# Kernel tuning notes

Measured on AMD Instinct MI355X. Metric: run time of the kernel, lower is better.

Reference implementation:

```python
import jax, jax.numpy as jnp
import numpy as np

N_QUBITS = 4
DIM = 2 ** N_QUBITS  # 16-dim statevector
KERNEL = 3
STRIDE = 1
PADDING = 1


def _rot_mats(w):
    # PennyLane Rot(phi, theta, omega) = RZ(omega) RY(theta) RZ(phi)
    phi, theta, omega = w[:, 0], w[:, 1], w[:, 2]
    c = jnp.cos(theta / 2)
    s = jnp.sin(theta / 2)
    em = jnp.exp(-0.5j * (phi + omega))
    ep = jnp.exp(0.5j * (phi + omega))
    ed = jnp.exp(0.5j * (phi - omega))
    edm = jnp.exp(-0.5j * (phi - omega))
    row0 = jnp.stack([em * c, -ed * s], axis=-1)
    row1 = jnp.stack([edm * s, ep * c], axis=-1)
    return jnp.stack([row0, row1], axis=-2)  # [n_qubits, 2, 2]


def _apply_1q(state, U, wire):
    # state: [M] + [2]*n, wire axis is 1+wire (wire 0 is most significant)
    s = jnp.moveaxis(state, 1 + wire, -1)
    s = jnp.einsum('...b,ab->...a', s, U)
    return jnp.moveaxis(s, -1, 1 + wire)


def _apply_cnot(state, c, t):
    s = jnp.moveaxis(state, (1 + c, 1 + t), (-2, -1))
    shp = s.shape
    s = s.reshape(shp[:-2] + (4,))[..., jnp.array([0, 1, 3, 2])].reshape(shp)
    return jnp.moveaxis(s, (-2, -1), (1 + c, 1 + t))


def _forward(x, W_pre, b_pre, W_post, b_post, q_weights):
    B, C, L = x.shape
    xp = jnp.pad(x, ((0, 0), (0, 0), (PADDING, PADDING)))
    L_out = (L + 2 * PADDING - KERNEL) // STRIDE + 1
    starts = jnp.arange(L_out) * STRIDE
    # windows: [B, C, L_out, K] -> flatten channel-major like torch reshape
    win = xp[:, :, starts[:, None] + jnp.arange(KERNEL)[None, :]]
    win = win.transpose(0, 2, 1, 3).reshape(B, L_out, C * KERNEL)
    pre = win @ W_pre.T + b_pre  # [B, L_out, n_qubits]
    # AmplitudeEmbedding: pad to 2**n and normalize
    v = jnp.pad(pre, ((0, 0), (0, 0), (0, DIM - N_QUBITS)))
    v = v / jnp.linalg.norm(v, axis=-1, keepdims=True)
    state = v.reshape(B * L_out, *([2] * N_QUBITS)).astype(jnp.complex64)
    U = _rot_mats(q_weights)
    for i in range(N_QUBITS):
        state = _apply_1q(state, U[i], i)
    for i in range(N_QUBITS - 1):
        state = _apply_cnot(state, i, i + 1)
    flat = state.reshape(B * L_out, DIM)
    probs = jnp.real(flat) ** 2 + jnp.imag(flat) ** 2
    # PauliZ expectation per wire: sign of bit i (wire 0 = MSB)
    bits = (jnp.arange(DIM)[None, :] >> (N_QUBITS - 1 - jnp.arange(N_QUBITS)[:, None])) & 1
    z = (1 - 2 * bits).astype(probs.dtype)  # [n_qubits, DIM]
    expz = (probs @ z.T).reshape(B, L_out, N_QUBITS)
    out = expz @ W_post.T + b_post  # [B, L_out, out_channels]
    return out.transpose(0, 2, 1)


def setup_inputs() -> dict:
    key = jax.random.key(0)
    ks = jax.random.split(key, 6)
    B, C, L = 32, 80, 3000
    OUT = 512
    return {
        'x': jax.random.normal(ks[0], (B, C, L), dtype=jnp.float32),
        'W_pre': jax.random.normal(ks[1], (N_QUBITS, C * KERNEL), dtype=jnp.float32) * 0.06,
        'b_pre': jax.random.normal(ks[2], (N_QUBITS,), dtype=jnp.float32) * 0.06,
        'W_post': jax.random.normal(ks[3], (OUT, N_QUBITS), dtype=jnp.float32) * 0.4,
        'b_post': jax.random.normal(ks[4], (OUT,), dtype=jnp.float32) * 0.4,
        'q_weights': jax.random.normal(ks[5], (N_QUBITS, 3), dtype=jnp.float32),
    }


def reference(x, W_pre, b_pre, W_post, b_post, q_weights):
    return _forward(x, W_pre, b_pre, W_post, b_post, q_weights)
```

## Files before the change

### kernel.cpp

```cpp
#include <hip/hip_runtime.h>
#include <math.h>

#define C_IN 80
#define L_IN 3000
#define OUT_C 512
#define TL1 128
#define NT1 256
#define NT2 256
#define TL2 256
#define OH  256

struct c2f { float x, y; };

__device__ __forceinline__ c2f cmul(c2f a, c2f b) {
    return { a.x*b.x - a.y*b.y, a.x*b.y + a.y*b.x };
}
__device__ __forceinline__ c2f csel(c2f a, c2f b, int bit) {
    c2f r; r.x = bit ? b.x : a.x; r.y = bit ? b.y : a.y; return r;
}
__device__ __forceinline__ float quadform(const float4* __restrict__ A, float4 p) {
    float4 r0 = A[0], r1 = A[1], r2 = A[2], r3 = A[3];
    return p.x*(r0.x*p.x + r0.y*p.y + r0.z*p.z + r0.w*p.w)
         + p.y*(r1.x*p.x + r1.y*p.y + r1.z*p.z + r1.w*p.w)
         + p.z*(r2.x*p.x + r2.y*p.y + r2.z*p.z + r2.w*p.w)
         + p.w*(r3.x*p.x + r3.y*p.y + r3.z*p.z + r3.w*p.w);
}

__global__ __launch_bounds__(NT1) void qconv_expz_kernel(
    const float* __restrict__ x,
    const float* __restrict__ W_pre,
    const float* __restrict__ b_pre,
    const float* __restrict__ qw,
    float4* __restrict__ expz)
{
    __shared__ float4 s_wpre[C_IN*3];
    __shared__ float4 s_A[4][4];
    __shared__ float4 s_part[TL1];

    const int t  = threadIdx.x;
    const int b  = blockIdx.y;
    const int l0 = blockIdx.x * TL1;

    for (int i = t; i < C_IN*3; i += NT1) {
        s_wpre[i] = make_float4(W_pre[0*C_IN*3 + i], W_pre[1*C_IN*3 + i],
                                W_pre[2*C_IN*3 + i], W_pre[3*C_IN*3 + i]);
    }
    __syncthreads();

    if (t < 64) {
        c2f U[4][2][2];
        #pragma unroll
        for (int i = 0; i < 4; ++i) {
            float phi = qw[i*3+0], theta = qw[i*3+1], omega = qw[i*3+2];
            float sh, ch;  sincosf(0.5f*theta, &sh, &ch);
            float s1, c1;  sincosf(0.5f*(phi+omega), &s1, &c1);
            float s2, cv;  sincosf(0.5f*(phi-omega), &s2, &cv);
            U[i][0][0] = {  c1*ch, -s1*ch };
            U[i][0][1] = { -cv*sh, -s2*sh };
            U[i][1][0] = {  cv*sh, -s2*sh };
            U[i][1][1] = {  c1*ch,  s1*ch };
        }
        const int q  = t >> 4;
        const int j  = (t >> 2) & 3;
        const int jp = t & 3;
        const int j2  = (j  >> 1) & 1, j3  = j  & 1;
        const int jp2 = (jp >> 1) & 1, jp3 = jp & 1;
        float s = 0.f;
        #pragma unroll
        for (int k = 0; k < 16; ++k) {
            int m = k ^ ((k >> 1) & 1);
            m ^= ((m >> 2) & 1) << 1;
            m ^= ((m >> 3) & 1) << 2;
            const int m0 = (m >> 3) & 1, m1 = (m >> 2) & 1;
            const int m2 = (m >> 1) & 1, m3 = m & 1;
            c2f w01 = cmul(U[0][m0][0], U[1][m1][0]);
            c2f av = cmul(w01, cmul(csel(U[2][m2][0], U[2][m2][1], j2),
                                    csel(U[3][m3][0], U[3][m3][1], j3)));
            c2f bv = cmul(w01, cmul(csel(U[2][m2][0], U[2][m2][1], jp2),
                                    csel(U[3][m3][0], U[3][m3][1], jp3)));
            float z = 1.f - 2.f * ((k >> (3 - q)) & 1);
            s += z * (av.x*bv.x + av.y*bv.y);
        }
        ((float*)s_A)[t] = s;
    }

    const int i = t & (TL1 - 1);
    const int h = t >> 7;
    const int l = l0 + i;
    const bool lvalid = (l < L_IN);

    float4 acc = (h == 0) ? make_float4(b_pre[0], b_pre[1], b_pre[2], b_pre[3])
                          : make_float4(0.f, 0.f, 0.f, 0.f);
    if (lvalid) {
        const float* __restrict__ xrow = x + (size_t)b * C_IN * L_IN + (size_t)(h*40) * L_IN + l;
        const bool has_m1 = (l >= 1);
        const bool has_p1 = (l + 1 < L_IN);
        #pragma unroll 4
        for (int c = 0; c < 40; ++c) {
            const float* r = xrow + c * L_IN;
            float xa = has_m1 ? r[-1] : 0.f;
            float xb = r[0];
            float xc = has_p1 ? r[1] : 0.f;
            float4 w0 = s_wpre[(h*40+c)*3+0], w1 = s_wpre[(h*40+c)*3+1], w2 = s_wpre[(h*40+c)*3+2];
            acc.x += w0.x*xa + w1.x*xb + w2.x*xc;
            acc.y += w0.y*xa + w1.y*xb + w2.y*xc;
            acc.z += w0.z*xa + w1.z*xb + w2.z*xc;
            acc.w += w0.w*xa + w1.w*xb + w2.w*xc;
        }
    }
    if (h == 1) s_part[i] = acc;
    __syncthreads();

    if (t < TL1 && lvalid) {
        float4 p = acc;
        float4 q2 = s_part[t];
        p.x += q2.x; p.y += q2.y; p.z += q2.z; p.w += q2.w;
        const float inv = 1.f / (p.x*p.x + p.y*p.y + p.z*p.z + p.w*p.w);
        float4 e;
        e.x = quadform(s_A[0], p) * inv;
        e.y = quadform(s_A[1], p) * inv;
        e.z = quadform(s_A[2], p) * inv;
        e.w = quadform(s_A[3], p) * inv;
        expz[(size_t)b * L_IN + l] = e;
    }
}

__global__ __launch_bounds__(NT2) void expand_kernel(
    const float4* __restrict__ expz,
    const float* __restrict__ W_post,
    const float* __restrict__ b_post,
    float* __restrict__ out)
{
    __shared__ float4 s_post[OH];
    __shared__ float  s_bpost[OH];

    const int t  = threadIdx.x;
    const int b  = blockIdx.z;
    const int oh = blockIdx.y;
    const int l0 = blockIdx.x * TL2;

    const int obase = oh * OH;
    s_post[t]  = *reinterpret_cast<const float4*>(&W_post[(obase + t) * 4]);
    s_bpost[t] = b_post[obase + t];

    const int lane = t & 63;
    const int w    = t >> 6;
    const int l    = l0 + 4 * lane;
    const bool v   = (l + 3 < L_IN);

    float4 e0, e1, e2, e3;
    if (v) {
        const float4* ep = expz + (size_t)b * L_IN + l;
        e0 = ep[0]; e1 = ep[1]; e2 = ep[2]; e3 = ep[3];
    }
    __syncthreads();
    if (!v) return;

    float* op = out + (size_t)b * OUT_C * L_IN + (size_t)(obase + w) * L_IN + l;
    #pragma unroll 8
    for (int k = 0; k < OH/4; ++k) {
        const int o = w + 4*k;
        const float4 wv = s_post[o];
        const float  bb = s_bpost[o];
        float4 st;
        st.x = wv.x*e0.x + wv.y*e0.y + wv.z*e0.z + wv.w*e0.w + bb;
        st.y = wv.x*e1.x + wv.y*e1.y + wv.z*e1.z + wv.w*e1.w + bb;
        st.z = wv.x*e2.x + wv.y*e2.y + wv.z*e2.z + wv.w*e2.w + bb;
        st.w = wv.x*e3.x + wv.y*e3.y + wv.z*e3.z + wv.w*e3.w + bb;
        *reinterpret_cast<float4*>(op) = st;
        op += (size_t)4 * L_IN;
    }
}

extern "C" void kernel_launch(void* const* d_in, const int* in_sizes, int n_in,
                              void* d_out, int out_size, void* d_ws, size_t ws_size,
                              hipStream_t stream) {
    const float* x      = (const float*)d_in[0];
    const float* W_pre  = (const float*)d_in[1];
    const float* b_pre  = (const float*)d_in[2];
    const float* W_post = (const float*)d_in[3];
    const float* b_post = (const float*)d_in[4];
    const float* qw     = (const float*)d_in[5];
    float* out = (float*)d_out;
    float4* expz = (float4*)d_ws;

    const int B = in_sizes[0] / (C_IN * L_IN);
    dim3 grid1((L_IN + TL1 - 1) / TL1, B);
    qconv_expz_kernel<<<grid1, NT1, 0, stream>>>(x, W_pre, b_pre, qw, expz);
    dim3 grid2((L_IN + TL2 - 1) / TL2, OUT_C / OH, B);
    expand_kernel<<<grid2, NT2, 0, stream>>>(expz, W_post, b_post, out);
}
```

Measured before the change: 49.42 us.

## Restructure expand kernel to stage full expz row in LDS with register-held weights

The expand kernel now gives each block 32 output channels for one batch. It loads the whole batch row of expz (3000 float4, 48KB) into shared memory, and each wave keeps 8 weight rows and biases in registers. Every wave sweeps the full length and writes 8 output rows per iteration. This removes the per-element shared-memory weight reads and the remainder handling. In exchange it uses 48KB of LDS per block, which lowers occupancy, and 3000 (not a multiple of 4) relies on the l<L_IN guard for the last float4.

```diff
diff --git a/kernel.cpp b/kernel.cpp
--- a/kernel.cpp
+++ b/kernel.cpp
@@ -7,8 +7,8 @@
 #define TL1 128
 #define NT1 256
 #define NT2 256
-#define TL2 256
-#define OH  256
+
+typedef float floatx4 __attribute__((ext_vector_type(4)));
 
 struct c2f { float x, y; };
 
@@ -34,7 +34,7 @@
     float4* __restrict__ expz)
 {
     __shared__ float4 s_wpre[C_IN*3];
-    __shared__ float4 s_A[4][4];
+    __shared__ float4 s_A[16];
     __shared__ float4 s_part[TL1];
 
     const int t  = threadIdx.x;
@@ -117,10 +117,10 @@
         p.x += q2.x; p.y += q2.y; p.z += q2.z; p.w += q2.w;
         const float inv = 1.f / (p.x*p.x + p.y*p.y + p.z*p.z + p.w*p.w);
         float4 e;
-        e.x = quadform(s_A[0], p) * inv;
-        e.y = quadform(s_A[1], p) * inv;
-        e.z = quadform(s_A[2], p) * inv;
-        e.w = quadform(s_A[3], p) * inv;
+        e.x = quadform(&s_A[0],  p) * inv;
+        e.y = quadform(&s_A[4],  p) * inv;
+        e.z = quadform(&s_A[8],  p) * inv;
+        e.w = quadform(&s_A[12], p) * inv;
         expz[(size_t)b * L_IN + l] = e;
     }
 }
@@ -131,44 +131,45 @@
     const float* __restrict__ b_post,
     float* __restrict__ out)
 {
-    __shared__ float4 s_post[OH];
-    __shared__ float  s_bpost[OH];
+    __shared__ float4 s_e[L_IN];
 
-    const int t  = threadIdx.x;
-    const int b  = blockIdx.z;
-    const int oh = blockIdx.y;
-    const int l0 = blockIdx.x * TL2;
+    const int t    = threadIdx.x;
+    const int og   = blockIdx.x;
+    const int b    = blockIdx.y;
+    const int w    = t >> 6;
+    const int lane = t & 63;
 
-    const int obase = oh * OH;
-    s_post[t]  = *reinterpret_cast<const float4*>(&W_post[(obase + t) * 4]);
-    s_bpost[t] = b_post[obase + t];
+    const float4* ep = expz + (size_t)b * L_IN;
+    for (int i = t; i < L_IN; i += NT2) s_e[i] = ep[i];
 
-    const int lane = t & 63;
-    const int w    = t >> 6;
-    const int l    = l0 + 4 * lane;
-    const bool v   = (l + 3 < L_IN);
-
-    float4 e0, e1, e2, e3;
-    if (v) {
-        const float4* ep = expz + (size_t)b * L_IN + l;
-        e0 = ep[0]; e1 = ep[1]; e2 = ep[2]; e3 = ep[3];
+    const int obase = og*32 + w*8;
+    float4 wv[8]; float bb[8];
+    #pragma unroll
+    for (int r = 0; r < 8; ++r) {
+        wv[r] = *reinterpret_cast<const float4*>(&W_post[(obase + r) * 4]);
+        bb[r] = b_post[obase + r];
     }
     __syncthreads();
-    if (!v) return;
 
-    float* op = out + (size_t)b * OUT_C * L_IN + (size_t)(obase + w) * L_IN + l;
-    #pragma unroll 8
-    for (int k = 0; k < OH/4; ++k) {
-        const int o = w + 4*k;
-        const float4 wv = s_post[o];
-        const float  bb = s_bpost[o];
-        float4 st;
-        st.x = wv.x*e0.x + wv.y*e0.y + wv.z*e0.z + wv.w*e0.w + bb;
-        st.y = wv.x*e1.x + wv.y*e1.y + wv.z*e1.z + wv.w*e1.w + bb;
-        st.z = wv.x*e2.x + wv.y*e2.y + wv.z*e2.z + wv.w*e2.w + bb;
-        st.w = wv.x*e3.x + wv.y*e3.y + wv.z*e3.z + wv.w*e3.w + bb;
-        *reinterpret_cast<float4*>(op) = st;
-        op += (size_t)4 * L_IN;
+    float* orow = out + ((size_t)b * OUT_C + obase) * L_IN;
+    #pragma unroll 2
+    for (int it = 0; it < (L_IN + 255) / 256; ++it) {
+        const int l = it*256 + lane*4;
+        if (l < L_IN) {
+            const float4 e0 = s_e[l+0];
+            const float4 e1 = s_e[l+1];
+            const float4 e2 = s_e[l+2];
+            const float4 e3 = s_e[l+3];
+            #pragma unroll
+            for (int r = 0; r < 8; ++r) {
+                floatx4 st;
+                st.x = wv[r].x*e0.x + wv[r].y*e0.y + wv[r].z*e0.z + wv[r].w*e0.w + bb[r];
+                st.y = wv[r].x*e1.x + wv[r].y*e1.y + wv[r].z*e1.z + wv[r].w*e1.w + bb[r];
+                st.z = wv[r].x*e2.x + wv[r].y*e2.y + wv[r].z*e2.z + wv[r].w*e2.w + bb[r];
+                st.w = wv[r].x*e3.x + wv[r].y*e3.y + wv[r].z*e3.z + wv[r].w*e3.w + bb[r];
+                *reinterpret_cast<floatx4*>(orow + (size_t)r * L_IN + l) = st;
+            }
+        }
     }
 }
 
@@ -187,6 +188,6 @@
     const int B = in_sizes[0] / (C_IN * L_IN);
     dim3 grid1((L_IN + TL1 - 1) / TL1, B);
     qconv_expz_kernel<<<grid1, NT1, 0, stream>>>(x, W_pre, b_pre, qw, expz);
-    dim3 grid2((L_IN + TL2 - 1) / TL2, OUT_C / OH, B);
+    dim3 grid2(OUT_C / 32, B);
     expand_kernel<<<grid2, NT2, 0, stream>>>(expz, W_post, b_post, out);
 }
```

Measured after the change: 50.37 us. About the same (+1.9%).
